# Performance work log

Hardware: AMD Instinct MI355X
Metric: run time of the kernel (lower is better)

Reference implementation:

```python
import jax, jax.numpy as jnp
import numpy as np

N_PROTS = 2048
MOLS_PER_PROT = 8
N_MOLS = N_PROTS * MOLS_PER_PROT
DIM = 768
MARGIN = 0.5


def setup_inputs() -> dict:
    key = jax.random.key(0)
    k1, k2, k3 = jax.random.split(key, 3)
    prot_emb = jax.random.normal(k1, (N_PROTS, DIM), dtype=jnp.float32)
    mol_emb = jax.random.normal(k2, (N_MOLS, DIM), dtype=jnp.float32)
    # L2-normalize like typical CLIP-style retrieval embeddings
    prot_emb = prot_emb / jnp.linalg.norm(prot_emb, axis=1, keepdims=True)
    mol_emb = mol_emb / jnp.linalg.norm(mol_emb, axis=1, keepdims=True)
    # block-structured labels: protein i paired with mols [8i, 8i+8)
    rows = jnp.repeat(jnp.arange(N_PROTS), MOLS_PER_PROT)
    cols = jnp.arange(N_MOLS)
    labels = jnp.zeros((N_PROTS, N_MOLS), dtype=jnp.float32).at[rows, cols].set(1.0)
    # pIC50 values in [2, 10]
    pic50_matrix = 2.0 + 8.0 * jax.random.uniform(k3, (N_PROTS, N_MOLS), dtype=jnp.float32)
    logit_scale = jnp.float32(1.0 / 0.07)
    return {"prot_emb": prot_emb, "mol_emb": mol_emb, "labels": labels,
            "pic50_matrix": pic50_matrix, "logit_scale": logit_scale}


def reference(prot_emb, mol_emb, labels, pic50_matrix, logit_scale):
    n_prots = prot_emb.shape[0]
    n_mols = mol_emb.shape[0]
    sim = jnp.matmul(prot_emb, mol_emb.T) * logit_scale  # [n_prots, n_mols]

    # affinity-weighted InfoNCE (prot -> mol)
    pic50_norm = jnp.clip((pic50_matrix - 2.0) / 8.0, 0.0, 1.0)
    pos_w = labels * pic50_norm
    pos_w = pos_w / (pos_w.sum(axis=1, keepdims=True) + 1e-8)
    loss_p2m = -jnp.sum(pos_w * jax.nn.log_softmax(sim, axis=1)) / n_prots

    # mol -> prot NLL
    mol_labels = jnp.argmax(labels, axis=0)  # [n_mols]
    lsm_m2p = jax.nn.log_softmax(sim.T, axis=1)  # [n_mols, n_prots]
    loss_m2p = -jnp.mean(lsm_m2p[jnp.arange(n_mols), mol_labels])

    # pairwise margin-ranking among positives (exactly MOLS_PER_PROT positives per protein)
    P = MOLS_PER_PROT
    _, pos_idx = jax.lax.top_k(labels, P)  # [n_prots, P] indices of positives
    pos_pic = jnp.take_along_axis(pic50_matrix, pos_idx, axis=1)  # [n_prots, P]
    pos_sc = jnp.take_along_axis(sim, pos_idx, axis=1)            # [n_prots, P]
    dp = pos_pic[:, :, None] - pos_pic[:, None, :]  # [n_prots, P, P]
    ds = pos_sc[:, :, None] - pos_sc[:, None, :]
    pair = jnp.where(dp > 0, jax.nn.relu(MARGIN - ds),
                     jnp.where(dp < 0, jax.nn.relu(MARGIN + ds), 0.0))
    upper = jnp.triu(jnp.ones((P, P), dtype=bool), k=1)  # unordered pairs j<k
    n_pairs = n_prots * (P * (P - 1) // 2)
    ranking_loss = jnp.sum(jnp.where(upper[None], pair, 0.0)) / n_pairs

    # negative push-down
    neg_loss = jnp.mean(jax.nn.relu(sim * (1.0 - labels)))

    total = loss_p2m + loss_m2p + 0.5 * ranking_loss + 0.1 * neg_loss
    return (total, loss_p2m, loss_m2p, ranking_loss, neg_loss)
```

## Files before the change

### kernel.cpp

```cpp
#include <hip/hip_runtime.h>
#include <hip/hip_bf16.h>
#include <math.h>

#define N_PROTS 2048
#define N_MOLS  16384
#define DIM     768
#define SHIFT   16.0f
#define MARGIN  0.5f

typedef __attribute__((ext_vector_type(8))) short short8;
typedef __attribute__((ext_vector_type(4))) float f32x4;
typedef __attribute__((ext_vector_type(4))) unsigned short us4;

__device__ __forceinline__ unsigned short bf16rnd(float x) {
    unsigned int u = __float_as_uint(x);
    u += 0x7fffu + ((u >> 16) & 1u);
    return (unsigned short)(u >> 16);
}


__global__ __launch_bounds__(256, 2)
void sim_pass(const float* __restrict__ prot, const float* __restrict__ mol,
              const float* __restrict__ scale_p,
              float* __restrict__ row_se, float* __restrict__ col_se,
              float* __restrict__ pos_sim, float* __restrict__ scalars)
{
    __shared__ unsigned short As[128][32];
    __shared__ unsigned short Bs[128][32];
    __shared__ float redBuf[4];

    const int tid = threadIdx.x;
    const int rowBase = blockIdx.y * 128;
    const int colBase = blockIdx.x * 128;

    const int wave = tid >> 6;
    const int lane = tid & 63;
    const int wr = (wave >> 1) * 64;
    const int wc = (wave & 1) * 64;
    const int l15 = lane & 15;
    const int q   = lane >> 4;

    f32x4 acc[4][4];
#pragma unroll
    for (int i = 0; i < 4; ++i)
#pragma unroll
        for (int j = 0; j < 4; ++j) acc[i][j] = (f32x4){0.f, 0.f, 0.f, 0.f};

    const float* aBase = prot + (size_t)rowBase * DIM;
    const float* bBase = mol  + (size_t)colBase * DIM;

    float4 aReg[4], bReg[4];

#pragma unroll
    for (int i = 0; i < 4; ++i) {
        int f = tid + 256 * i;
        int row = f >> 3, c4 = f & 7;
        aReg[i] = *(const float4*)(aBase + (size_t)row * DIM + (c4 << 2));
        bReg[i] = *(const float4*)(bBase + (size_t)row * DIM + (c4 << 2));
    }

#pragma unroll 1
    for (int s = 0; s < DIM / 32; ++s) {
#pragma unroll
        for (int i = 0; i < 4; ++i) {
            int f = tid + 256 * i;
            int row = f >> 3, c4 = f & 7;
            us4 av, bv;
            av.x = bf16rnd(aReg[i].x); av.y = bf16rnd(aReg[i].y);
            av.z = bf16rnd(aReg[i].z); av.w = bf16rnd(aReg[i].w);
            bv.x = bf16rnd(bReg[i].x); bv.y = bf16rnd(bReg[i].y);
            bv.z = bf16rnd(bReg[i].z); bv.w = bf16rnd(bReg[i].w);
            *(us4*)&As[row][c4 << 2] = av;
            *(us4*)&Bs[row][c4 << 2] = bv;
        }
        __syncthreads();

        if (s + 1 < DIM / 32) {
            int k0 = (s + 1) * 32;
#pragma unroll
            for (int i = 0; i < 4; ++i) {
                int f = tid + 256 * i;
                int row = f >> 3, c4 = f & 7;
                aReg[i] = *(const float4*)(aBase + (size_t)row * DIM + k0 + (c4 << 2));
                bReg[i] = *(const float4*)(bBase + (size_t)row * DIM + k0 + (c4 << 2));
            }
        }

        short8 aF[4], bF[4];
#pragma unroll
        for (int mi = 0; mi < 4; ++mi) aF[mi] = *(const short8*)&As[wr + mi * 16 + l15][q * 8];
#pragma unroll
        for (int ni = 0; ni < 4; ++ni) bF[ni] = *(const short8*)&Bs[wc + ni * 16 + l15][q * 8];
#pragma unroll
        for (int mi = 0; mi < 4; ++mi)
#pragma unroll
            for (int ni = 0; ni < 4; ++ni)
                acc[mi][ni] = __builtin_amdgcn_mfma_f32_16x16x32_bf16(aF[mi], bF[ni], acc[mi][ni], 0, 0, 0);
        __syncthreads();
    }

    const float scale = scale_p[0];
    float rsum[4][4];
    float csum[4] = {0.f, 0.f, 0.f, 0.f};
    float rl = 0.f;
#pragma unroll
    for (int mi = 0; mi < 4; ++mi)
#pragma unroll
        for (int r = 0; r < 4; ++r) rsum[mi][r] = 0.f;

#pragma unroll
    for (int mi = 0; mi < 4; ++mi) {
#pragma unroll
        for (int ni = 0; ni < 4; ++ni) {
#pragma unroll
            for (int r = 0; r < 4; ++r) {
                float sim = acc[mi][ni][r] * scale;
                float e = __expf(sim - SHIFT);
                rsum[mi][r] += e;
                csum[ni] += e;
                rl += fmaxf(sim, 0.f);
                int rg = rowBase + wr + mi * 16 + q * 4 + r;
                int cg = colBase + wc + ni * 16 + l15;
                if ((cg >> 3) == rg) pos_sim[cg] = sim;
            }
        }
    }

#pragma unroll
    for (int mi = 0; mi < 4; ++mi) {
#pragma unroll
        for (int r = 0; r < 4; ++r) {
            float v = rsum[mi][r];
            v += __shfl_xor(v, 1); v += __shfl_xor(v, 2);
            v += __shfl_xor(v, 4); v += __shfl_xor(v, 8);
            if (l15 == 0)
                atomicAdd(&row_se[rowBase + wr + mi * 16 + q * 4 + r], v);
        }
    }

#pragma unroll
    for (int ni = 0; ni < 4; ++ni) {
        float v = csum[ni];
        v += __shfl_xor(v, 16); v += __shfl_xor(v, 32);
        if (q == 0)
            atomicAdd(&col_se[colBase + wc + ni * 16 + l15], v);
    }

#pragma unroll
    for (int m = 1; m < 64; m <<= 1) rl += __shfl_xor(rl, m);
    if (lane == 0) redBuf[wave] = rl;
    __syncthreads();
    if (tid == 0)
        atomicAdd(&scalars[0], redBuf[0] + redBuf[1] + redBuf[2] + redBuf[3]);
}

__global__ __launch_bounds__(256)
void finalize1(const float* __restrict__ row_se, const float* __restrict__ col_se,
               const float* __restrict__ pos_sim, const float* __restrict__ pic50,
               float* __restrict__ scalars)
{
    int j = blockIdx.x * 256 + threadIdx.x;
    float m2p = SHIFT + __logf(col_se[j]) - pos_sim[j];

    float p2m = 0.f, rank = 0.f, prelu = 0.f;
    if ((j & 7) == 0) {
        int i = j >> 3;
        float s[8], pc[8], pr[8];
#pragma unroll
        for (int p = 0; p < 8; ++p) {
            s[p]  = pos_sim[j + p];
            pr[p] = pic50[(size_t)i * N_MOLS + j + p];
            float x = (pr[p] - 2.0f) * 0.125f;
            pc[p] = fminf(fmaxf(x, 0.f), 1.f);
            prelu += fmaxf(s[p], 0.f);
        }
        float wsum = 1e-8f;
#pragma unroll
        for (int p = 0; p < 8; ++p) wsum += pc[p];
        float lse = SHIFT + __logf(row_se[i]);
        float accp = 0.f;
#pragma unroll
        for (int p = 0; p < 8; ++p) accp += pc[p] * (lse - s[p]);
        p2m = accp / wsum;
#pragma unroll
        for (int a = 0; a < 8; ++a)
#pragma unroll
            for (int b = a + 1; b < 8; ++b) {
                float dp = pr[a] - pr[b];
                float ds = s[a] - s[b];
                float v = (dp > 0.f) ? fmaxf(MARGIN - ds, 0.f)
                        : ((dp < 0.f) ? fmaxf(MARGIN + ds, 0.f) : 0.f);
                rank += v;
            }
    }

#pragma unroll
    for (int m = 1; m < 64; m <<= 1) {
        m2p  += __shfl_xor(m2p, m);
        p2m  += __shfl_xor(p2m, m);
        rank += __shfl_xor(rank, m);
        prelu += __shfl_xor(prelu, m);
    }
    __shared__ float rbuf[4][4];
    int wave = threadIdx.x >> 6, lane = threadIdx.x & 63;
    if (lane == 0) { rbuf[wave][0] = m2p; rbuf[wave][1] = p2m; rbuf[wave][2] = rank; rbuf[wave][3] = prelu; }
    __syncthreads();
    if (threadIdx.x == 0) {
        float a = 0, b = 0, c = 0, d = 0;
        for (int w = 0; w < 4; ++w) { a += rbuf[w][0]; b += rbuf[w][1]; c += rbuf[w][2]; d += rbuf[w][3]; }
        atomicAdd(&scalars[2], a);
        atomicAdd(&scalars[1], b);
        atomicAdd(&scalars[3], c);
        atomicAdd(&scalars[4], d);
    }
}

__global__ void finalize2(const float* __restrict__ scalars, float* __restrict__ out)
{
    float relu_neg = scalars[0] - scalars[4];
    float p2m  = scalars[1] / (float)N_PROTS;
    float m2p  = scalars[2] / (float)N_MOLS;
    float rank = scalars[3] / ((float)N_PROTS * 28.0f);
    float neg  = relu_neg / ((float)N_PROTS * (float)N_MOLS);
    out[0] = p2m + m2p + 0.5f * rank + 0.1f * neg;
    out[1] = p2m;
    out[2] = m2p;
    out[3] = rank;
    out[4] = neg;
}

extern "C" void kernel_launch(void* const* d_in, const int* in_sizes, int n_in,
                              void* d_out, int out_size, void* d_ws, size_t ws_size,
                              hipStream_t stream) {
    const float* prot   = (const float*)d_in[0];
    const float* mol    = (const float*)d_in[1];
    const float* pic50  = (const float*)d_in[3];
    const float* lscale = (const float*)d_in[4];

    float* ws      = (float*)d_ws;
    float* row_se  = ws;
    float* col_se  = ws + 2048;
    float* pos_sim = ws + 2048 + 16384;
    float* scalars = ws + 2048 + 16384 + 16384;

    hipMemsetAsync(d_ws, 0, (size_t)(2048 + 16384 + 16384 + 8) * sizeof(float), stream);

    dim3 grid(N_MOLS / 128, N_PROTS / 128);
    sim_pass<<<grid, 256, 0, stream>>>(prot, mol, lscale, row_se, col_se, pos_sim, scalars);
    finalize1<<<N_MOLS / 256, 256, 0, stream>>>(row_se, col_se, pos_sim, pic50, scalars);
    finalize2<<<1, 1, 0, stream>>>(scalars, (float*)d_out);
}
```

Measured before the change: 402.3 us.

## Pre-convert embeddings to bf16 and stream tiles via global_load_lds

Adds a pre-pass that converts protein and molecule embeddings to bf16 in workspace. A new GEMM kernel then loads bf16 tiles straight into LDS with global_load_lds, removing per-tile fp32 loads and in-loop rounding. This halves the bytes each tile reloads from global memory. The cost is an extra kernel launch plus a full write and read of bf16 copies, and the new main loop has no register prefetch, so it relies on occupancy to hide load latency. The old path is kept as a fallback when the workspace is too small.

Measured after the change: 395.3 us. No clear change (-1.7%).

```diff
diff --git a/kernel.cpp b/kernel.cpp
--- a/kernel.cpp
+++ b/kernel.cpp
@@ -11,6 +11,7 @@
 typedef __attribute__((ext_vector_type(8))) short short8;
 typedef __attribute__((ext_vector_type(4))) float f32x4;
 typedef __attribute__((ext_vector_type(4))) unsigned short us4;
+typedef __attribute__((ext_vector_type(8))) unsigned short us8;
 
 __device__ __forceinline__ unsigned short bf16rnd(float x) {
     unsigned int u = __float_as_uint(x);
@@ -18,12 +19,101 @@
     return (unsigned short)(u >> 16);
 }
 
+__device__ __forceinline__ void gload16(const void* g, void* l) {
+    __builtin_amdgcn_global_load_lds(
+        (const __attribute__((address_space(1))) unsigned int*)g,
+        (__attribute__((address_space(3))) unsigned int*)l, 16, 0, 0);
+}
+
+#define ACC_FLOATS 34824
+#define PROT_BF_OFF_B 139296ull
+#define PROT_BF_BYTES (2048ull*768*2)
+#define MOL_BF_OFF_B  (PROT_BF_OFF_B + PROT_BF_BYTES)
+#define MOL_BF_BYTES  (16384ull*768*2)
+#define WS_NEED       (MOL_BF_OFF_B + MOL_BF_BYTES)
+
+__global__ __launch_bounds__(256)
+void convert_bf16(const float* __restrict__ prot, const float* __restrict__ mol,
+                  unsigned short* __restrict__ protBf, unsigned short* __restrict__ molBf)
+{
+    const size_t PROT_G = (size_t)N_PROTS * DIM / 8;
+    size_t t = (size_t)blockIdx.x * 256 + threadIdx.x;
+    const float* src;
+    unsigned short* dst;
+    if (t < PROT_G) { src = prot + t * 8; dst = protBf + t * 8; }
+    else            { size_t u = t - PROT_G; src = mol + u * 8; dst = molBf + u * 8; }
+    float4 v0 = ((const float4*)src)[0];
+    float4 v1 = ((const float4*)src)[1];
+    us8 o;
+    o[0] = bf16rnd(v0.x); o[1] = bf16rnd(v0.y); o[2] = bf16rnd(v0.z); o[3] = bf16rnd(v0.w);
+    o[4] = bf16rnd(v1.x); o[5] = bf16rnd(v1.y); o[6] = bf16rnd(v1.z); o[7] = bf16rnd(v1.w);
+    *(us8*)dst = o;
+}
+
+__device__ __forceinline__ void epilogue(
+    f32x4 acc[4][4], float scale, int rowBase, int colBase,
+    int wave, int lane, int wr, int wc, int l15, int q,
+    float* __restrict__ row_se, float* __restrict__ col_se,
+    float* __restrict__ pos_sim, float* __restrict__ scalars, float* redBuf)
+{
+    float rsum[4][4];
+    float csum[4] = {0.f, 0.f, 0.f, 0.f};
+    float rl = 0.f;
+#pragma unroll
+    for (int mi = 0; mi < 4; ++mi)
+#pragma unroll
+        for (int r = 0; r < 4; ++r) rsum[mi][r] = 0.f;
+
+#pragma unroll
+    for (int mi = 0; mi < 4; ++mi) {
+#pragma unroll
+        for (int ni = 0; ni < 4; ++ni) {
+#pragma unroll
+            for (int r = 0; r < 4; ++r) {
+                float sim = acc[mi][ni][r] * scale;
+                float e = __expf(sim - SHIFT);
+                rsum[mi][r] += e;
+                csum[ni] += e;
+                rl += fmaxf(sim, 0.f);
+                int rg = rowBase + wr + mi * 16 + q * 4 + r;
+                int cg = colBase + wc + ni * 16 + l15;
+                if ((cg >> 3) == rg) pos_sim[cg] = sim;
+            }
+        }
+    }
+
+#pragma unroll
+    for (int mi = 0; mi < 4; ++mi) {
+#pragma unroll
+        for (int r = 0; r < 4; ++r) {
+            float v = rsum[mi][r];
+            v += __shfl_xor(v, 1); v += __shfl_xor(v, 2);
+            v += __shfl_xor(v, 4); v += __shfl_xor(v, 8);
+            if (l15 == 0)
+                atomicAdd(&row_se[rowBase + wr + mi * 16 + q * 4 + r], v);
+        }
+    }
+#pragma unroll
+    for (int ni = 0; ni < 4; ++ni) {
+        float v = csum[ni];
+        v += __shfl_xor(v, 16); v += __shfl_xor(v, 32);
+        if (q == 0)
+            atomicAdd(&col_se[colBase + wc + ni * 16 + l15], v);
+    }
+#pragma unroll
+    for (int m = 1; m < 64; m <<= 1) rl += __shfl_xor(rl, m);
+    if (lane == 0) redBuf[wave] = rl;
+    __syncthreads();
+    if (wave == 0 && lane == 0)
+        atomicAdd(&scalars[0], redBuf[0] + redBuf[1] + redBuf[2] + redBuf[3]);
+}
 
 __global__ __launch_bounds__(256, 2)
-void sim_pass(const float* __restrict__ prot, const float* __restrict__ mol,
-              const float* __restrict__ scale_p,
-              float* __restrict__ row_se, float* __restrict__ col_se,
-              float* __restrict__ pos_sim, float* __restrict__ scalars)
+void sim_pass_bf16(const unsigned short* __restrict__ protBf,
+                   const unsigned short* __restrict__ molBf,
+                   const float* __restrict__ scale_p,
+                   float* __restrict__ row_se, float* __restrict__ col_se,
+                   float* __restrict__ pos_sim, float* __restrict__ scalars)
 {
     __shared__ unsigned short As[128][32];
     __shared__ unsigned short Bs[128][32];
@@ -32,7 +122,6 @@
     const int tid = threadIdx.x;
     const int rowBase = blockIdx.y * 128;
     const int colBase = blockIdx.x * 128;
-
     const int wave = tid >> 6;
     const int lane = tid & 63;
     const int wr = (wave >> 1) * 64;
@@ -46,11 +135,70 @@
 #pragma unroll
         for (int j = 0; j < 4; ++j) acc[i][j] = (f32x4){0.f, 0.f, 0.f, 0.f};
 
+    const int subRow = tid >> 2;
+    const int subCol = (tid & 3) << 3;
+    const unsigned short* aP0 = protBf + (size_t)(rowBase + subRow) * DIM + subCol;
+    const unsigned short* aP1 = aP0 + (size_t)64 * DIM;
+    const unsigned short* bP0 = molBf + (size_t)(colBase + subRow) * DIM + subCol;
+    const unsigned short* bP1 = bP0 + (size_t)64 * DIM;
+    unsigned short* ldsA = &As[0][0] + (wave << 9);
+    unsigned short* ldsB = &Bs[0][0] + (wave << 9);
+
+#pragma unroll 1
+    for (int s = 0; s < DIM / 32; ++s) {
+        gload16(aP0, ldsA);
+        gload16(aP1, ldsA + 2048);
+        gload16(bP0, ldsB);
+        gload16(bP1, ldsB + 2048);
+        aP0 += 32; aP1 += 32; bP0 += 32; bP1 += 32;
+        __syncthreads();
+
+        short8 aF[4], bF[4];
+#pragma unroll
+        for (int mi = 0; mi < 4; ++mi) aF[mi] = *(const short8*)&As[wr + mi * 16 + l15][q * 8];
+#pragma unroll
+        for (int ni = 0; ni < 4; ++ni) bF[ni] = *(const short8*)&Bs[wc + ni * 16 + l15][q * 8];
+#pragma unroll
+        for (int mi = 0; mi < 4; ++mi)
+#pragma unroll
+            for (int ni = 0; ni < 4; ++ni)
+                acc[mi][ni] = __builtin_amdgcn_mfma_f32_16x16x32_bf16(aF[mi], bF[ni], acc[mi][ni], 0, 0, 0);
+        __syncthreads();
+    }
+
+    epilogue(acc, scale_p[0], rowBase, colBase, wave, lane, wr, wc, l15, q,
+             row_se, col_se, pos_sim, scalars, redBuf);
+}
+
+__global__ __launch_bounds__(256, 2)
+void sim_pass(const float* __restrict__ prot, const float* __restrict__ mol,
+              const float* __restrict__ scale_p,
+              float* __restrict__ row_se, float* __restrict__ col_se,
+              float* __restrict__ pos_sim, float* __restrict__ scalars)
+{
+    __shared__ unsigned short As[128][32];
+    __shared__ unsigned short Bs[128][32];
+    __shared__ float redBuf[4];
+
+    const int tid = threadIdx.x;
+    const int rowBase = blockIdx.y * 128;
+    const int colBase = blockIdx.x * 128;
+    const int wave = tid >> 6;
+    const int lane = tid & 63;
+    const int wr = (wave >> 1) * 64;
+    const int wc = (wave & 1) * 64;
+    const int l15 = lane & 15;
+    const int q   = lane >> 4;
+
+    f32x4 acc[4][4];
+#pragma unroll
+    for (int i = 0; i < 4; ++i)
+#pragma unroll
+        for (int j = 0; j < 4; ++j) acc[i][j] = (f32x4){0.f, 0.f, 0.f, 0.f};
+
     const float* aBase = prot + (size_t)rowBase * DIM;
     const float* bBase = mol  + (size_t)colBase * DIM;
-
     float4 aReg[4], bReg[4];
-
 #pragma unroll
     for (int i = 0; i < 4; ++i) {
         int f = tid + 256 * i;
@@ -58,7 +206,6 @@
         aReg[i] = *(const float4*)(aBase + (size_t)row * DIM + (c4 << 2));
         bReg[i] = *(const float4*)(bBase + (size_t)row * DIM + (c4 << 2));
     }
-
 #pragma unroll 1
     for (int s = 0; s < DIM / 32; ++s) {
 #pragma unroll
@@ -74,7 +221,6 @@
             *(us4*)&Bs[row][c4 << 2] = bv;
         }
         __syncthreads();
-
         if (s + 1 < DIM / 32) {
             int k0 = (s + 1) * 32;
 #pragma unroll
@@ -85,7 +231,6 @@
                 bReg[i] = *(const float4*)(bBase + (size_t)row * DIM + k0 + (c4 << 2));
             }
         }
-
         short8 aF[4], bF[4];
 #pragma unroll
         for (int mi = 0; mi < 4; ++mi) aF[mi] = *(const short8*)&As[wr + mi * 16 + l15][q * 8];
@@ -99,59 +244,8 @@
         __syncthreads();
     }
 
-    const float scale = scale_p[0];
-    float rsum[4][4];
-    float csum[4] = {0.f, 0.f, 0.f, 0.f};
-    float rl = 0.f;
-#pragma unroll
-    for (int mi = 0; mi < 4; ++mi)
-#pragma unroll
-        for (int r = 0; r < 4; ++r) rsum[mi][r] = 0.f;
-
-#pragma unroll
-    for (int mi = 0; mi < 4; ++mi) {
-#pragma unroll
-        for (int ni = 0; ni < 4; ++ni) {
-#pragma unroll
-            for (int r = 0; r < 4; ++r) {
-                float sim = acc[mi][ni][r] * scale;
-                float e = __expf(sim - SHIFT);
-                rsum[mi][r] += e;
-                csum[ni] += e;
-                rl += fmaxf(sim, 0.f);
-                int rg = rowBase + wr + mi * 16 + q * 4 + r;
-                int cg = colBase + wc + ni * 16 + l15;
-                if ((cg >> 3) == rg) pos_sim[cg] = sim;
-            }
-        }
-    }
-
-#pragma unroll
-    for (int mi = 0; mi < 4; ++mi) {
-#pragma unroll
-        for (int r = 0; r < 4; ++r) {
-            float v = rsum[mi][r];
-            v += __shfl_xor(v, 1); v += __shfl_xor(v, 2);
-            v += __shfl_xor(v, 4); v += __shfl_xor(v, 8);
-            if (l15 == 0)
-                atomicAdd(&row_se[rowBase + wr + mi * 16 + q * 4 + r], v);
-        }
-    }
-
-#pragma unroll
-    for (int ni = 0; ni < 4; ++ni) {
-        float v = csum[ni];
-        v += __shfl_xor(v, 16); v += __shfl_xor(v, 32);
-        if (q == 0)
-            atomicAdd(&col_se[colBase + wc + ni * 16 + l15], v);
-    }
-
-#pragma unroll
-    for (int m = 1; m < 64; m <<= 1) rl += __shfl_xor(rl, m);
-    if (lane == 0) redBuf[wave] = rl;
-    __syncthreads();
-    if (tid == 0)
-        atomicAdd(&scalars[0], redBuf[0] + redBuf[1] + redBuf[2] + redBuf[3]);
+    epilogue(acc, scale_p[0], rowBase, colBase, wave, lane, wr, wc, l15, q,
+             row_se, col_se, pos_sim, scalars, redBuf);
 }
 
 __global__ __launch_bounds__(256)
@@ -196,9 +290,9 @@
 
 #pragma unroll
     for (int m = 1; m < 64; m <<= 1) {
-        m2p  += __shfl_xor(m2p, m);
-        p2m  += __shfl_xor(p2m, m);
-        rank += __shfl_xor(rank, m);
+        m2p   += __shfl_xor(m2p, m);
+        p2m   += __shfl_xor(p2m, m);
+        rank  += __shfl_xor(rank, m);
         prelu += __shfl_xor(prelu, m);
     }
     __shared__ float rbuf[4][4];
@@ -243,10 +337,18 @@
     float* pos_sim = ws + 2048 + 16384;
     float* scalars = ws + 2048 + 16384 + 16384;
 
-    hipMemsetAsync(d_ws, 0, (size_t)(2048 + 16384 + 16384 + 8) * sizeof(float), stream);
+    hipMemsetAsync(d_ws, 0, (size_t)ACC_FLOATS * sizeof(float), stream);
 
     dim3 grid(N_MOLS / 128, N_PROTS / 128);
-    sim_pass<<<grid, 256, 0, stream>>>(prot, mol, lscale, row_se, col_se, pos_sim, scalars);
+    if (ws_size >= WS_NEED) {
+        unsigned short* protBf = (unsigned short*)((char*)d_ws + PROT_BF_OFF_B);
+        unsigned short* molBf  = (unsigned short*)((char*)d_ws + MOL_BF_OFF_B);
+        size_t groups = ((size_t)N_PROTS + N_MOLS) * DIM / 8;
+        convert_bf16<<<(unsigned)(groups / 256), 256, 0, stream>>>(prot, mol, protBf, molBf);
+        sim_pass_bf16<<<grid, 256, 0, stream>>>(protBf, molBf, lscale, row_se, col_se, pos_sim, scalars);
+    } else {
+        sim_pass<<<grid, 256, 0, stream>>>(prot, mol, lscale, row_se, col_se, pos_sim, scalars);
+    }
     finalize1<<<N_MOLS / 256, 256, 0, stream>>>(row_se, col_se, pos_sim, pic50, scalars);
     finalize2<<<1, 1, 0, stream>>>(scalars, (float*)d_out);
 }
```
